# Optimization experiments

Measured on AMD Instinct MI355X. Metric: run time of the kernel, lower is better.

The kernel has to match this reference:

```python
import jax, jax.numpy as jnp
import numpy as np

C = 256
RED = 2
C2 = C // RED


def setup_inputs() -> dict:
    key = jax.random.key(0)
    ks = jax.random.split(key, 6)
    B, H, W = 8, 64, 64
    x = jax.random.normal(ks[0], (B, C, H, W), dtype=jnp.float32)
    # 1x1 convs stored as [out_ch, in_ch] matrices
    W1 = jax.random.normal(ks[1], (C2, C), dtype=jnp.float32) * (1.0 / np.sqrt(C))
    b1 = jax.random.normal(ks[2], (C2,), dtype=jnp.float32) * 0.01
    W2 = jax.random.normal(ks[3], (C, C2), dtype=jnp.float32) * (1.0 / np.sqrt(C2))
    b2 = jax.random.normal(ks[4], (C,), dtype=jnp.float32) * 0.01
    # torch inits scale to zeros; use randn so the residual branch is active
    scale = jax.random.normal(ks[5], (1, C, 1, 1), dtype=jnp.float32)
    return {"x": x, "W1": W1, "b1": b1, "W2": W2, "b2": b2, "scale": scale}


def reference(x, W1, b1, W2, b2, scale):
    B, Cc, H, Wd = x.shape
    # conv1 (1x1): [B,C,H,W] -> [B,C2,H,W]
    y = jnp.einsum('bchw,oc->bohw', x, W1) + b1[None, :, None, None]
    # flatten spatial, move channels last: [B, N, C2]
    y = y.reshape(B, C2, H * Wd).transpose(0, 2, 1)
    # unscaled self-attention over N spatial positions
    att = jax.nn.softmax(jnp.einsum('bmc,bnc->bmn', y, y), axis=-1)  # [B,N,N]
    out = jnp.einsum('bmn,bnc->bmc', att, y)  # [B,N,C2]
    # faithful to torch: raw .view(B,-1,H,W) WITHOUT permuting back
    out = out.reshape(B, C2, H, Wd)
    # conv2 (1x1): [B,C2,H,W] -> [B,C,H,W]
    out = jnp.einsum('bchw,oc->bohw', out, W2) + b2[None, :, None, None]
    return out * scale + x
```

## Files before the change

### kernel.cpp

```cpp
#include <hip/hip_runtime.h>

#define B_  8
#define C_  256
#define C2_ 128
#define N_  4096
#define LOG2E 1.44269504088896f

typedef _Float16 f16;
typedef _Float16 f16x4 __attribute__((ext_vector_type(4)));
typedef _Float16 f16x8 __attribute__((ext_vector_type(8)));
typedef float f32x4  __attribute__((ext_vector_type(4)));

static __device__ __forceinline__ unsigned pk2(float a, float b) {
  return __builtin_bit_cast(unsigned, __builtin_amdgcn_cvt_pkrtz(a, b));
}

static __device__ __forceinline__ void plane16_swap(unsigned a, unsigned b,
                                                    unsigned& r0, unsigned& r1) {
#if __has_builtin(__builtin_amdgcn_permlane16_swap)
  auto r = __builtin_amdgcn_permlane16_swap(a, b, false, false);
  r0 = (unsigned)r[0]; r1 = (unsigned)r[1];
#else
  asm volatile("v_permlane16_swap_b32 %0, %1" : "+v"(a), "+v"(b));
  r0 = a; r1 = b;
#endif
}

static __device__ __forceinline__ void gload16(const void* g, void* l) {
  __builtin_amdgcn_global_load_lds(
      (const __attribute__((address_space(1))) unsigned int*)g,
      (__attribute__((address_space(3))) unsigned int*)l, 16, 0, 0);
}

__global__ __launch_bounds__(256)
void prep_kernel(const float* __restrict__ W1, const float* __restrict__ W2,
                 f16* __restrict__ w1h, f16* __restrict__ w2h)
{
  int i = blockIdx.x * 256 + threadIdx.x;
  w1h[i] = (f16)W1[i];
  w2h[i] = (f16)W2[i];
}

__global__ __launch_bounds__(256, 3)
void conv1_kernel(const float* __restrict__ x,
                  const f16* __restrict__ w1h,
                  const float* __restrict__ b1,
                  f16* __restrict__ Y, f16* __restrict__ Yt)
{
  __shared__ __align__(16) char smem[32768];
  f16* Xh = (f16*)smem;
  f16* Ah = (f16*)(smem + 16384);
  f16* T  = (f16*)smem;

  const int t = threadIdx.x;
  const int w = t >> 6, lane = t & 63, quad = lane >> 4, l16 = lane & 15;
  const int b = blockIdx.x, nt0 = blockIdx.y;

#pragma unroll
  for (int pass = 0; pass < 8; pass++) {
    int c  = (t >> 3) + pass * 32;
    int n4 = t & 7;
    float4 v = *(const float4*)(x + ((long)(b * C_ + c)) * N_ + nt0 * 32 + n4 * 4);
    f16x4 h = {(f16)v.x, (f16)v.y, (f16)v.z, (f16)v.w};
    *(f16x4*)(&Xh[c * 32 + (n4 ^ (c & 7)) * 4]) = h;
  }
  __syncthreads();
#pragma unroll
  for (int pass = 0; pass < 4; pass++) {
    int n  = t & 31;
    int kb = (t >> 5) + pass * 8;
    f16x8 vh;
#pragma unroll
    for (int jj = 0; jj < 8; jj++) {
      int cc = kb * 8 + jj;
      vh[jj] = Xh[cc * 32 + ((n >> 2) ^ (cc & 7)) * 4 + (n & 3)];
    }
    *(f16x8*)(&Ah[n * 256 + (kb ^ (n & 7)) * 8]) = vh;
  }
  __syncthreads();

  f16x8 bh[2][8];
#pragma unroll
  for (int nt = 0; nt < 2; nt++) {
    int c2 = w * 32 + nt * 16 + l16;
#pragma unroll
    for (int ks = 0; ks < 8; ks++)
      bh[nt][ks] = *(const f16x8*)(w1h + c2 * C_ + ks * 32 + quad * 8);
  }

  f32x4 acc[2][2];
#pragma unroll
  for (int i = 0; i < 2; i++)
#pragma unroll
    for (int j = 0; j < 2; j++) acc[i][j] = (f32x4){0.f, 0.f, 0.f, 0.f};

#pragma unroll
  for (int ks = 0; ks < 8; ks++)
#pragma unroll
    for (int mt = 0; mt < 2; mt++) {
      f16x8 ah = *(const f16x8*)(&Ah[(mt * 16 + l16) * 256 + (((ks * 4 + quad) ^ (l16 & 7))) * 8]);
#pragma unroll
      for (int nt = 0; nt < 2; nt++)
        acc[mt][nt] = __builtin_amdgcn_mfma_f32_16x16x32_f16(ah, bh[nt][ks], acc[mt][nt], 0, 0, 0);
    }
  __syncthreads();

#pragma unroll
  for (int nt = 0; nt < 2; nt++) {
    int c2 = w * 32 + nt * 16 + l16;
    float bv = b1[c2];
#pragma unroll
    for (int mt = 0; mt < 2; mt++)
#pragma unroll
      for (int rg = 0; rg < 4; rg++) {
        int n = mt * 16 + quad * 4 + rg;
        T[c2 * 40 + n] = (f16)(acc[mt][nt][rg] + bv);
      }
  }
  __syncthreads();
#pragma unroll
  for (int pass = 0; pass < 2; pass++) {
    int r  = (t >> 2) + pass * 64;
    int c8 = (t & 3) * 8;
    f16x8 v = *(const f16x8*)(&T[r * 40 + c8]);
    *(f16x8*)(Yt + ((long)(b * C2_ + r)) * N_ + nt0 * 32 + c8) = v;
  }
#pragma unroll
  for (int pass = 0; pass < 2; pass++) {
    int row = t & 31;
    int cg  = (t >> 5) + pass * 8;
    f16x8 v;
#pragma unroll
    for (int jj = 0; jj < 8; jj++) v[jj] = T[(cg * 8 + jj) * 40 + row];
    *(f16x8*)(Y + ((long)(b * N_ + nt0 * 32 + row)) * C2_ + cg * 8) = v;
  }
}

__global__ __launch_bounds__(256, 2)
void attn_kernel(const f16* __restrict__ Y, const f16* __restrict__ Yt,
                 f16* __restrict__ Op, float* __restrict__ ls)
{
  __shared__ f16 Ks[2][64 * 128];
  __shared__ f16 Vs[2][128 * 64];
  __shared__ float nsqf[128];

  const int t = threadIdx.x;
  const int w = t >> 6, lane = t & 63, quad = lane >> 4, l16 = lane & 15;
  const int b = blockIdx.x, qt = blockIdx.y, s = blockIdx.z;
  const int ns = gridDim.z;
  const f16* Yb  = Y  + (long)b * N_ * C2_;
  const f16* Ytb = Yt + (long)b * C2_ * N_;
  const int g0 = (s * 64) / ns;
  const int g1 = ((s + 1) * 64) / ns;

  int koff[4], voff[4];
#pragma unroll
  for (int i = 0; i < 4; i++) {
    int p = w + 4 * i;
    int r = 4 * p + (lane >> 4);
    koff[i] = r * C2_ + ((l16 ^ (r & 15)) * 8);
    int d = 8 * p + (lane >> 3);
    voff[i] = d * N_ + (((lane & 7) ^ (d & 7)) * 8);
  }

  f16x8 qf[2][4];
#pragma unroll
  for (int mt = 0; mt < 2; mt++)
#pragma unroll
    for (int ks = 0; ks < 4; ks++)
      qf[mt][ks] = *(const f16x8*)(Yb + (long)(qt * 128 + w * 32 + mt * 16 + l16) * C2_ + ks * 32 + quad * 8);

  {
    int r = t >> 1, half = t & 1;
    float ss = 0.f;
#pragma unroll
    for (int j = 0; j < 8; j++) {
      f16x8 v = *(const f16x8*)(Yb + (long)(qt * 128 + r) * C2_ + half * 64 + j * 8);
#pragma unroll
      for (int e = 0; e < 8; e++) { float f = (float)v[e]; ss = fmaf(f, f, ss); }
    }
    ss += __shfl_xor(ss, 1);
    if (!half) nsqf[r] = ss;
  }

  {
    const int kb0 = g0 * 64;
    const f16* gk = Yb + (long)kb0 * C2_;
    const f16* gv = Ytb + kb0;
#pragma unroll
    for (int i = 0; i < 4; i++) {
      gload16(gk + koff[i], &Ks[0][(w + 4 * i) * 512]);
      gload16(gv + voff[i], &Vs[0][(w + 4 * i) * 512]);
    }
  }
  __syncthreads();

  float nm[2];
  nm[0] = nsqf[w * 32 + l16] * LOG2E;
  nm[1] = nsqf[w * 32 + 16 + l16] * LOG2E;

  f16x8 ones8;
#pragma unroll
  for (int j = 0; j < 8; j++) ones8[j] = (f16)1.0f;

  f32x4 Oa[2][8];
#pragma unroll
  for (int i = 0; i < 2; i++)
#pragma unroll
    for (int j = 0; j < 8; j++) Oa[i][j] = (f32x4){0.f, 0.f, 0.f, 0.f};
  f32x4 lac[2] = {(f32x4){0.f,0.f,0.f,0.f}, (f32x4){0.f,0.f,0.f,0.f}};

  int cur = 0;
#pragma unroll 1
  for (int g = g0; g < g1; g++) {
    if (g + 1 < g1) {
      int nb = (g + 1) * 64;
      const f16* gk = Yb + (long)nb * C2_;
      const f16* gv = Ytb + nb;
#pragma unroll
      for (int i = 0; i < 4; i++) {
        gload16(gk + koff[i], &Ks[cur ^ 1][(w + 4 * i) * 512]);
        gload16(gv + voff[i], &Vs[cur ^ 1][(w + 4 * i) * 512]);
      }
    }

    f32x4 S[4][2];
#pragma unroll
    for (int i = 0; i < 4; i++)
#pragma unroll
      for (int j = 0; j < 2; j++) S[i][j] = (f32x4){0.f, 0.f, 0.f, 0.f};
#pragma unroll
    for (int ks = 0; ks < 4; ks++) {
      f16x8 b0 = *(const f16x8*)(&Ks[cur][(0 * 16 + l16) * 128 + (((ks * 4 + quad) ^ l16)) * 8]);
      f16x8 b1 = *(const f16x8*)(&Ks[cur][(1 * 16 + l16) * 128 + (((ks * 4 + quad) ^ l16)) * 8]);
      __builtin_amdgcn_s_setprio(1);
#pragma unroll
      for (int mt = 0; mt < 2; mt++) {
        S[0][mt] = __builtin_amdgcn_mfma_f32_16x16x32_f16(b0, qf[mt][ks], S[0][mt], 0, 0, 0);
        S[1][mt] = __builtin_amdgcn_mfma_f32_16x16x32_f16(b1, qf[mt][ks], S[1][mt], 0, 0, 0);
      }
      __builtin_amdgcn_s_setprio(0);
    }
#pragma unroll
    for (int ks = 0; ks < 4; ks++) {
      f16x8 b2 = *(const f16x8*)(&Ks[cur][(2 * 16 + l16) * 128 + (((ks * 4 + quad) ^ l16)) * 8]);
      f16x8 b3 = *(const f16x8*)(&Ks[cur][(3 * 16 + l16) * 128 + (((ks * 4 + quad) ^ l16)) * 8]);
      __builtin_amdgcn_s_setprio(1);
#pragma unroll
      for (int mt = 0; mt < 2; mt++) {
        S[2][mt] = __builtin_amdgcn_mfma_f32_16x16x32_f16(b2, qf[mt][ks], S[2][mt], 0, 0, 0);
        S[3][mt] = __builtin_amdgcn_mfma_f32_16x16x32_f16(b3, qf[mt][ks], S[3][mt], 0, 0, 0);
      }
      __builtin_amdgcn_s_setprio(0);
    }

    f16x8 pa0[2];
#pragma unroll
    for (int mt = 0; mt < 2; mt++) {
      float n0 = nm[mt];
      unsigned xa0 = pk2(exp2f(fminf(fmaf(S[0][mt][0], LOG2E, -n0), 11.0f)),
                         exp2f(fminf(fmaf(S[0][mt][1], LOG2E, -n0), 11.0f)));
      unsigned xa1 = pk2(exp2f(fminf(fmaf(S[0][mt][2], LOG2E, -n0), 11.0f)),
                         exp2f(fminf(fmaf(S[0][mt][3], LOG2E, -n0), 11.0f)));
      unsigned xb0 = pk2(exp2f(fminf(fmaf(S[1][mt][0], LOG2E, -n0), 11.0f)),
                         exp2f(fminf(fmaf(S[1][mt][1], LOG2E, -n0), 11.0f)));
      unsigned xb1 = pk2(exp2f(fminf(fmaf(S[1][mt][2], LOG2E, -n0), 11.0f)),
                         exp2f(fminf(fmaf(S[1][mt][3], LOG2E, -n0), 11.0f)));
      union { unsigned u[4]; f16x8 v; } P;
      {
        auto c = __builtin_amdgcn_permlane32_swap(xa0, xb0, false, false);
        plane16_swap((unsigned)c[0], (unsigned)c[1], P.u[0], P.u[2]);
      }
      {
        auto c = __builtin_amdgcn_permlane32_swap(xa1, xb1, false, false);
        plane16_swap((unsigned)c[0], (unsigned)c[1], P.u[1], P.u[3]);
      }
      pa0[mt] = P.v;
    }

    {
      f16x8 vb[8];
#pragma unroll
      for (int dt = 0; dt < 8; dt++)
        vb[dt] = *(const f16x8*)(&Vs[cur][(dt * 16 + l16) * 64 + (((0 * 4 + quad) ^ (l16 & 7))) * 8]);
      __builtin_amdgcn_s_setprio(1);
#pragma unroll
      for (int mt = 0; mt < 2; mt++) {
#pragma unroll
        for (int dt = 0; dt < 8; dt++)
          Oa[mt][dt] = __builtin_amdgcn_mfma_f32_16x16x32_f16(pa0[mt], vb[dt], Oa[mt][dt], 0, 0, 0);
        lac[mt] = __builtin_amdgcn_mfma_f32_16x16x32_f16(pa0[mt], ones8, lac[mt], 0, 0, 0);
      }
      __builtin_amdgcn_s_setprio(0);
    }

    f16x8 pa1[2];
#pragma unroll
    for (int mt = 0; mt < 2; mt++) {
      float n0 = nm[mt];
      unsigned xa0 = pk2(exp2f(fminf(fmaf(S[2][mt][0], LOG2E, -n0), 11.0f)),
                         exp2f(fminf(fmaf(S[2][mt][1], LOG2E, -n0), 11.0f)));
      unsigned xa1 = pk2(exp2f(fminf(fmaf(S[2][mt][2], LOG2E, -n0), 11.0f)),
                         exp2f(fminf(fmaf(S[2][mt][3], LOG2E, -n0), 11.0f)));
      unsigned xb0 = pk2(exp2f(fminf(fmaf(S[3][mt][0], LOG2E, -n0), 11.0f)),
                         exp2f(fminf(fmaf(S[3][mt][1], LOG2E, -n0), 11.0f)));
      unsigned xb1 = pk2(exp2f(fminf(fmaf(S[3][mt][2], LOG2E, -n0), 11.0f)),
                         exp2f(fminf(fmaf(S[3][mt][3], LOG2E, -n0), 11.0f)));
      union { unsigned u[4]; f16x8 v; } P;
      {
        auto c = __builtin_amdgcn_permlane32_swap(xa0, xb0, false, false);
        plane16_swap((unsigned)c[0], (unsigned)c[1], P.u[0], P.u[2]);
      }
      {
        auto c = __builtin_amdgcn_permlane32_swap(xa1, xb1, false, false);
        plane16_swap((unsigned)c[0], (unsigned)c[1], P.u[1], P.u[3]);
      }
      pa1[mt] = P.v;
    }

    {
      f16x8 vb[8];
#pragma unroll
      for (int dt = 0; dt < 8; dt++)
        vb[dt] = *(const f16x8*)(&Vs[cur][(dt * 16 + l16) * 64 + (((1 * 4 + quad) ^ (l16 & 7))) * 8]);
      __builtin_amdgcn_s_setprio(1);
#pragma unroll
      for (int mt = 0; mt < 2; mt++) {
#pragma unroll
        for (int dt = 0; dt < 8; dt++)
          Oa[mt][dt] = __builtin_amdgcn_mfma_f32_16x16x32_f16(pa1[mt], vb[dt], Oa[mt][dt], 0, 0, 0);
        lac[mt] = __builtin_amdgcn_mfma_f32_16x16x32_f16(pa1[mt], ones8, lac[mt], 0, 0, 0);
      }
      __builtin_amdgcn_s_setprio(0);
    }

    __syncthreads();
    cur ^= 1;
  }

  const long rbase = ((long)s * B_ + b) * N_ + qt * 128;
#pragma unroll
  for (int mt = 0; mt < 2; mt++)
#pragma unroll
    for (int rg = 0; rg < 4; rg++) {
      int r = w * 32 + mt * 16 + quad * 4 + rg;
#pragma unroll
      for (int dt = 0; dt < 8; dt++)
        Op[(rbase + r) * C2_ + dt * 16 + l16] = (f16)Oa[mt][dt][rg];
      if (l16 == 0) ls[rbase + r] = lac[mt][rg];
    }
}

__global__ __launch_bounds__(256, 4)
void conv2_kernel(const f16* __restrict__ Op, const float* __restrict__ ls,
                  const f16* __restrict__ w2h,
                  const float* __restrict__ b2,
                  const float* __restrict__ scale,
                  const float* __restrict__ x,
                  float* __restrict__ out, int ns)
{
  __shared__ __align__(16) char smem2[35328];
  f16*   Or   = (f16*)smem2;
  f16*   Bsw  = (f16*)(smem2 + 18432);
  float* invL = (float*)(smem2 + 34816);
  float* Obuf = (float*)smem2;

  const int t = threadIdx.x;
  const int w = t >> 6, lane = t & 63, quad = lane >> 4, l16 = lane & 15;
  const int b = blockIdx.x, pt = blockIdx.y, oh = blockIdx.z;
  const long base0 = (long)b * 524288;

  if (t < 128) {
    int q = t * 32 + (pt >> 1);
    float l = 0.f;
    for (int si = 0; si < ns; si++)
      l += ls[(long)si * 32768 + (long)b * N_ + q];
    invL[t] = 1.0f / fmaxf(l, 1e-20f);
  }
  __syncthreads();

#pragma unroll
  for (int pass = 0; pass < 4; pass++) {
    int j = (t >> 3) + pass * 32;
    int c8 = (t & 7) * 8;
    float fa[8] = {0.f,0.f,0.f,0.f,0.f,0.f,0.f,0.f};
    for (int si = 0; si < ns; si++) {
      f16x8 a = *(const f16x8*)(Op + (long)si * 4194304 + base0 + (long)j * N_ + pt * 64 + c8);
#pragma unroll
      for (int jj = 0; jj < 8; jj++) fa[jj] += (float)a[jj];
    }
    float iv = invL[j];
    f16x8 r;
#pragma unroll
    for (int jj = 0; jj < 8; jj++)
      r[jj] = (f16)(fa[jj] * iv);
    *(f16x8*)(&Or[j * 72 + c8]) = r;
  }
  __syncthreads();
#pragma unroll
  for (int pass = 0; pass < 4; pass++) {
    int p = t & 63;
    int q = (t >> 6) + pass * 4;
    f16x8 vv;
#pragma unroll
    for (int jj = 0; jj < 8; jj++) vv[jj] = Or[(q * 8 + jj) * 72 + p];
    *(f16x8*)(&Bsw[p * 128 + ((q ^ (p & 15))) * 8]) = vv;
  }
  __syncthreads();

  f32x4 acc[2][4];
#pragma unroll
  for (int i = 0; i < 2; i++)
#pragma unroll
    for (int j = 0; j < 4; j++) acc[i][j] = (f32x4){0.f, 0.f, 0.f, 0.f};

#pragma unroll
  for (int ks = 0; ks < 4; ks++) {
    f16x8 bfr[4];
#pragma unroll
    for (int nt = 0; nt < 4; nt++)
      bfr[nt] = *(const f16x8*)(&Bsw[(nt * 16 + l16) * 128 + (((ks * 4 + quad) ^ l16)) * 8]);
#pragma unroll
    for (int mt = 0; mt < 2; mt++) {
      int o = oh * 128 + w * 32 + mt * 16 + l16;
      f16x8 ah = *(const f16x8*)(w2h + o * C2_ + ks * 32 + quad * 8);
#pragma unroll
      for (int nt = 0; nt < 4; nt++)
        acc[mt][nt] = __builtin_amdgcn_mfma_f32_16x16x32_f16(ah, bfr[nt], acc[mt][nt], 0, 0, 0);
    }
  }

  __syncthreads();
#pragma unroll
  for (int mt = 0; mt < 2; mt++)
#pragma unroll
    for (int nt = 0; nt < 4; nt++)
#pragma unroll
      for (int rg = 0; rg < 4; rg++)
        Obuf[(w * 32 + mt * 16 + quad * 4 + rg) * 68 + nt * 16 + l16] = acc[mt][nt][rg];
  __syncthreads();
#pragma unroll
  for (int pass = 0; pass < 8; pass++) {
    int idx = pass * 256 + t;
    int ol  = idx >> 4;
    int p4  = (idx & 15) * 4;
    float4 v = *(const float4*)(&Obuf[ol * 68 + p4]);
    int o = oh * 128 + ol;
    float so = scale[o], bo = b2[o];
    long xo = ((long)b * C_ + o) * N_ + pt * 64 + p4;
    float4 xv = *(const float4*)(x + xo);
    float4 r;
    r.x = (v.x + bo) * so + xv.x;
    r.y = (v.y + bo) * so + xv.y;
    r.z = (v.z + bo) * so + xv.z;
    r.w = (v.w + bo) * so + xv.w;
    *(float4*)(out + xo) = r;
  }
}

extern "C" void kernel_launch(void* const* d_in, const int* in_sizes, int n_in,
                              void* d_out, int out_size, void* d_ws, size_t ws_size,
                              hipStream_t stream) {
  const float* x     = (const float*)d_in[0];
  const float* W1    = (const float*)d_in[1];
  const float* b1    = (const float*)d_in[2];
  const float* W2    = (const float*)d_in[3];
  const float* b2    = (const float*)d_in[4];
  const float* scale = (const float*)d_in[5];
  float* outp = (float*)d_out;

  const size_t NE = (size_t)B_ * N_ * C2_;
  const int ns = 2;

  f16* Y   = (f16*)d_ws;
  f16* Yt  = Y + NE;
  f16* Op  = Yt + NE;
  float* ls = (float*)(Op + (size_t)ns * NE);
  f16* w1h = (f16*)(ls + (size_t)ns * 32768);
  f16* w2h = w1h + 32768;

  prep_kernel <<<dim3(128),       dim3(256), 0, stream>>>(W1, W2, w1h, w2h);
  conv1_kernel<<<dim3(8, 128),    dim3(256), 0, stream>>>(x, w1h, b1, Y, Yt);
  attn_kernel <<<dim3(8, 32, ns), dim3(256), 0, stream>>>(Y, Yt, Op, ls);
  conv2_kernel<<<dim3(8, 64, 2),  dim3(256), 0, stream>>>(Op, ls, w2h, b2, scale, x, outp, ns);
}
```

Before: 208.6 us.

## Software-pipeline QK and PV across key tiles; merge conv2 output halves per block

The attention loop now computes QK^T for tile i while running the PV MFMAs of tile i-1, using stored P fragments. K is loaded one tile ahead and V is loaded for the current tile into alternating buffers, with a drain step after the loop. The aim is to overlap the softmax exp work with matrix-core work. Separately, conv2 loops over both output-channel halves inside one block, so the partial-output merge and transpose are done once instead of twice. This doubles the block's LDS and halves the grid. Register pressure rises in attention, and conv2 occupancy drops.

```diff
diff --git a/kernel.cpp b/kernel.cpp
--- a/kernel.cpp
+++ b/kernel.cpp
@@ -152,6 +152,7 @@
   const f16* Ytb = Yt + (long)b * C2_ * N_;
   const int g0 = (s * 64) / ns;
   const int g1 = ((s + 1) * 64) / ns;
+  const int nt_ = g1 - g0;
 
   int koff[4], voff[4];
 #pragma unroll
@@ -184,14 +185,10 @@
   }
 
   {
-    const int kb0 = g0 * 64;
-    const f16* gk = Yb + (long)kb0 * C2_;
-    const f16* gv = Ytb + kb0;
-#pragma unroll
-    for (int i = 0; i < 4; i++) {
+    const f16* gk = Yb + (long)(g0 * 64) * C2_;
+#pragma unroll
+    for (int i = 0; i < 4; i++)
       gload16(gk + koff[i], &Ks[0][(w + 4 * i) * 512]);
-      gload16(gv + voff[i], &Vs[0][(w + 4 * i) * 512]);
-    }
   }
   __syncthreads();
 
@@ -210,132 +207,109 @@
     for (int j = 0; j < 8; j++) Oa[i][j] = (f32x4){0.f, 0.f, 0.f, 0.f};
   f32x4 lac[2] = {(f32x4){0.f,0.f,0.f,0.f}, (f32x4){0.f,0.f,0.f,0.f}};
 
-  int cur = 0;
+  f16x8 pa_prev[2][2];
+
 #pragma unroll 1
-  for (int g = g0; g < g1; g++) {
-    if (g + 1 < g1) {
-      int nb = (g + 1) * 64;
-      const f16* gk = Yb + (long)nb * C2_;
-      const f16* gv = Ytb + nb;
-#pragma unroll
-      for (int i = 0; i < 4; i++) {
-        gload16(gk + koff[i], &Ks[cur ^ 1][(w + 4 * i) * 512]);
-        gload16(gv + voff[i], &Vs[cur ^ 1][(w + 4 * i) * 512]);
+  for (int i = 0; i < nt_; i++) {
+    const int g = g0 + i;
+    const int kb = i & 1;
+
+    if (i + 1 < nt_) {
+      const f16* gk = Yb + (long)((g + 1) * 64) * C2_;
+#pragma unroll
+      for (int j = 0; j < 4; j++)
+        gload16(gk + koff[j], &Ks[kb ^ 1][(w + 4 * j) * 512]);
+    }
+    {
+      const f16* gv = Ytb + g * 64;
+#pragma unroll
+      for (int j = 0; j < 4; j++)
+        gload16(gv + voff[j], &Vs[kb][(w + 4 * j) * 512]);
+    }
+
+    f32x4 S[4][2];
+#pragma unroll
+    for (int a = 0; a < 4; a++)
+#pragma unroll
+      for (int j = 0; j < 2; j++) S[a][j] = (f32x4){0.f, 0.f, 0.f, 0.f};
+#pragma unroll
+    for (int ks = 0; ks < 4; ks++) {
+      f16x8 bfr[4];
+#pragma unroll
+      for (int nt = 0; nt < 4; nt++)
+        bfr[nt] = *(const f16x8*)(&Ks[kb][(nt * 16 + l16) * 128 + (((ks * 4 + quad) ^ l16)) * 8]);
+      __builtin_amdgcn_s_setprio(1);
+#pragma unroll
+      for (int nt = 0; nt < 4; nt++)
+#pragma unroll
+        for (int mt = 0; mt < 2; mt++)
+          S[nt][mt] = __builtin_amdgcn_mfma_f32_16x16x32_f16(bfr[nt], qf[mt][ks], S[nt][mt], 0, 0, 0);
+      __builtin_amdgcn_s_setprio(0);
+    }
+
+    if (i > 0) {
+#pragma unroll
+      for (int ks2 = 0; ks2 < 2; ks2++) {
+        f16x8 vb[8];
+#pragma unroll
+        for (int dt = 0; dt < 8; dt++)
+          vb[dt] = *(const f16x8*)(&Vs[kb ^ 1][(dt * 16 + l16) * 64 + (((ks2 * 4 + quad) ^ (l16 & 7))) * 8]);
+        __builtin_amdgcn_s_setprio(1);
+#pragma unroll
+        for (int mt = 0; mt < 2; mt++) {
+#pragma unroll
+          for (int dt = 0; dt < 8; dt++)
+            Oa[mt][dt] = __builtin_amdgcn_mfma_f32_16x16x32_f16(pa_prev[ks2][mt], vb[dt], Oa[mt][dt], 0, 0, 0);
+          lac[mt] = __builtin_amdgcn_mfma_f32_16x16x32_f16(pa_prev[ks2][mt], ones8, lac[mt], 0, 0, 0);
+        }
+        __builtin_amdgcn_s_setprio(0);
       }
     }
 
-    f32x4 S[4][2];
-#pragma unroll
-    for (int i = 0; i < 4; i++)
-#pragma unroll
-      for (int j = 0; j < 2; j++) S[i][j] = (f32x4){0.f, 0.f, 0.f, 0.f};
-#pragma unroll
-    for (int ks = 0; ks < 4; ks++) {
-      f16x8 b0 = *(const f16x8*)(&Ks[cur][(0 * 16 + l16) * 128 + (((ks * 4 + quad) ^ l16)) * 8]);
-      f16x8 b1 = *(const f16x8*)(&Ks[cur][(1 * 16 + l16) * 128 + (((ks * 4 + quad) ^ l16)) * 8]);
-      __builtin_amdgcn_s_setprio(1);
+#pragma unroll
+    for (int ks2 = 0; ks2 < 2; ks2++)
 #pragma unroll
       for (int mt = 0; mt < 2; mt++) {
-        S[0][mt] = __builtin_amdgcn_mfma_f32_16x16x32_f16(b0, qf[mt][ks], S[0][mt], 0, 0, 0);
-        S[1][mt] = __builtin_amdgcn_mfma_f32_16x16x32_f16(b1, qf[mt][ks], S[1][mt], 0, 0, 0);
+        float n0 = nm[mt];
+        unsigned xa0 = pk2(exp2f(fminf(fmaf(S[2 * ks2][mt][0], LOG2E, -n0), 11.0f)),
+                           exp2f(fminf(fmaf(S[2 * ks2][mt][1], LOG2E, -n0), 11.0f)));
+        unsigned xa1 = pk2(exp2f(fminf(fmaf(S[2 * ks2][mt][2], LOG2E, -n0), 11.0f)),
+                           exp2f(fminf(fmaf(S[2 * ks2][mt][3], LOG2E, -n0), 11.0f)));
+        unsigned xb0 = pk2(exp2f(fminf(fmaf(S[2 * ks2 + 1][mt][0], LOG2E, -n0), 11.0f)),
+                           exp2f(fminf(fmaf(S[2 * ks2 + 1][mt][1], LOG2E, -n0), 11.0f)));
+        unsigned xb1 = pk2(exp2f(fminf(fmaf(S[2 * ks2 + 1][mt][2], LOG2E, -n0), 11.0f)),
+                           exp2f(fminf(fmaf(S[2 * ks2 + 1][mt][3], LOG2E, -n0), 11.0f)));
+        union { unsigned u[4]; f16x8 v; } P;
+        {
+          auto c = __builtin_amdgcn_permlane32_swap(xa0, xb0, false, false);
+          plane16_swap((unsigned)c[0], (unsigned)c[1], P.u[0], P.u[2]);
+        }
+        {
+          auto c = __builtin_amdgcn_permlane32_swap(xa1, xb1, false, false);
+          plane16_swap((unsigned)c[0], (unsigned)c[1], P.u[1], P.u[3]);
+        }
+        pa_prev[ks2][mt] = P.v;
       }
-      __builtin_amdgcn_s_setprio(0);
-    }
-#pragma unroll
-    for (int ks = 0; ks < 4; ks++) {
-      f16x8 b2 = *(const f16x8*)(&Ks[cur][(2 * 16 + l16) * 128 + (((ks * 4 + quad) ^ l16)) * 8]);
-      f16x8 b3 = *(const f16x8*)(&Ks[cur][(3 * 16 + l16) * 128 + (((ks * 4 + quad) ^ l16)) * 8]);
-      __builtin_amdgcn_s_setprio(1);
+
+    __syncthreads();
+  }
+
+  {
+    const int kb = (nt_ - 1) & 1;
+#pragma unroll
+    for (int ks2 = 0; ks2 < 2; ks2++) {
+      f16x8 vb[8];
+#pragma unroll
+      for (int dt = 0; dt < 8; dt++)
+        vb[dt] = *(const f16x8*)(&Vs[kb][(dt * 16 + l16) * 64 + (((ks2 * 4 + quad) ^ (l16 & 7))) * 8]);
 #pragma unroll
       for (int mt = 0; mt < 2; mt++) {
-        S[2][mt] = __builtin_amdgcn_mfma_f32_16x16x32_f16(b2, qf[mt][ks], S[2][mt], 0, 0, 0);
-        S[3][mt] = __builtin_amdgcn_mfma_f32_16x16x32_f16(b3, qf[mt][ks], S[3][mt], 0, 0, 0);
+#pragma unroll
+        for (int dt = 0; dt < 8; dt++)
+          Oa[mt][dt] = __builtin_amdgcn_mfma_f32_16x16x32_f16(pa_prev[ks2][mt], vb[dt], Oa[mt][dt], 0, 0, 0);
+        lac[mt] = __builtin_amdgcn_mfma_f32_16x16x32_f16(pa_prev[ks2][mt], ones8, lac[mt], 0, 0, 0);
       }
-      __builtin_amdgcn_s_setprio(0);
-    }
-
-    f16x8 pa0[2];
-#pragma unroll
-    for (int mt = 0; mt < 2; mt++) {
-      float n0 = nm[mt];
-      unsigned xa0 = pk2(exp2f(fminf(fmaf(S[0][mt][0], LOG2E, -n0), 11.0f)),
-                         exp2f(fminf(fmaf(S[0][mt][1], LOG2E, -n0), 11.0f)));
-      unsigned xa1 = pk2(exp2f(fminf(fmaf(S[0][mt][2], LOG2E, -n0), 11.0f)),
-                         exp2f(fminf(fmaf(S[0][mt][3], LOG2E, -n0), 11.0f)));
-      unsigned xb0 = pk2(exp2f(fminf(fmaf(S[1][mt][0], LOG2E, -n0), 11.0f)),
-                         exp2f(fminf(fmaf(S[1][mt][1], LOG2E, -n0), 11.0f)));
-      unsigned xb1 = pk2(exp2f(fminf(fmaf(S[1][mt][2], LOG2E, -n0), 11.0f)),
-                         exp2f(fminf(fmaf(S[1][mt][3], LOG2E, -n0), 11.0f)));
-      union { unsigned u[4]; f16x8 v; } P;
-      {
-        auto c = __builtin_amdgcn_permlane32_swap(xa0, xb0, false, false);
-        plane16_swap((unsigned)c[0], (unsigned)c[1], P.u[0], P.u[2]);
-      }
-      {
-        auto c = __builtin_amdgcn_permlane32_swap(xa1, xb1, false, false);
-        plane16_swap((unsigned)c[0], (unsigned)c[1], P.u[1], P.u[3]);
-      }
-      pa0[mt] = P.v;
-    }
-
-    {
-      f16x8 vb[8];
-#pragma unroll
-      for (int dt = 0; dt < 8; dt++)
-        vb[dt] = *(const f16x8*)(&Vs[cur][(dt * 16 + l16) * 64 + (((0 * 4 + quad) ^ (l16 & 7))) * 8]);
-      __builtin_amdgcn_s_setprio(1);
-#pragma unroll
-      for (int mt = 0; mt < 2; mt++) {
-#pragma unroll
-        for (int dt = 0; dt < 8; dt++)
-          Oa[mt][dt] = __builtin_amdgcn_mfma_f32_16x16x32_f16(pa0[mt], vb[dt], Oa[mt][dt], 0, 0, 0);
-        lac[mt] = __builtin_amdgcn_mfma_f32_16x16x32_f16(pa0[mt], ones8, lac[mt], 0, 0, 0);
-      }
-      __builtin_amdgcn_s_setprio(0);
-    }
-
-    f16x8 pa1[2];
-#pragma unroll
-    for (int mt = 0; mt < 2; mt++) {
-      float n0 = nm[mt];
-      unsigned xa0 = pk2(exp2f(fminf(fmaf(S[2][mt][0], LOG2E, -n0), 11.0f)),
-                         exp2f(fminf(fmaf(S[2][mt][1], LOG2E, -n0), 11.0f)));
-      unsigned xa1 = pk2(exp2f(fminf(fmaf(S[2][mt][2], LOG2E, -n0), 11.0f)),
-                         exp2f(fminf(fmaf(S[2][mt][3], LOG2E, -n0), 11.0f)));
-      unsigned xb0 = pk2(exp2f(fminf(fmaf(S[3][mt][0], LOG2E, -n0), 11.0f)),
-                         exp2f(fminf(fmaf(S[3][mt][1], LOG2E, -n0), 11.0f)));
-      unsigned xb1 = pk2(exp2f(fminf(fmaf(S[3][mt][2], LOG2E, -n0), 11.0f)),
-                         exp2f(fminf(fmaf(S[3][mt][3], LOG2E, -n0), 11.0f)));
-      union { unsigned u[4]; f16x8 v; } P;
-      {
-        auto c = __builtin_amdgcn_permlane32_swap(xa0, xb0, false, false);
-        plane16_swap((unsigned)c[0], (unsigned)c[1], P.u[0], P.u[2]);
-      }
-      {
-        auto c = __builtin_amdgcn_permlane32_swap(xa1, xb1, false, false);
-        plane16_swap((unsigned)c[0], (unsigned)c[1], P.u[1], P.u[3]);
-      }
-      pa1[mt] = P.v;
-    }
-
-    {
-      f16x8 vb[8];
-#pragma unroll
-      for (int dt = 0; dt < 8; dt++)
-        vb[dt] = *(const f16x8*)(&Vs[cur][(dt * 16 + l16) * 64 + (((1 * 4 + quad) ^ (l16 & 7))) * 8]);
-      __builtin_amdgcn_s_setprio(1);
-#pragma unroll
-      for (int mt = 0; mt < 2; mt++) {
-#pragma unroll
-        for (int dt = 0; dt < 8; dt++)
-          Oa[mt][dt] = __builtin_amdgcn_mfma_f32_16x16x32_f16(pa1[mt], vb[dt], Oa[mt][dt], 0, 0, 0);
-        lac[mt] = __builtin_amdgcn_mfma_f32_16x16x32_f16(pa1[mt], ones8, lac[mt], 0, 0, 0);
-      }
-      __builtin_amdgcn_s_setprio(0);
-    }
-
-    __syncthreads();
-    cur ^= 1;
+    }
   }
 
   const long rbase = ((long)s * B_ + b) * N_ + qt * 128;
@@ -351,7 +325,7 @@
     }
 }
 
-__global__ __launch_bounds__(256, 4)
+__global__ __launch_bounds__(256, 2)
 void conv2_kernel(const f16* __restrict__ Op, const float* __restrict__ ls,
                   const f16* __restrict__ w2h,
                   const float* __restrict__ b2,
@@ -359,15 +333,15 @@
                   const float* __restrict__ x,
                   float* __restrict__ out, int ns)
 {
-  __shared__ __align__(16) char smem2[35328];
+  __shared__ __align__(16) char smem2[70144];
   f16*   Or   = (f16*)smem2;
   f16*   Bsw  = (f16*)(smem2 + 18432);
   float* invL = (float*)(smem2 + 34816);
-  float* Obuf = (float*)smem2;
+  float* Obuf = (float*)(smem2 + 35328);
 
   const int t = threadIdx.x;
   const int w = t >> 6, lane = t & 63, quad = lane >> 4, l16 = lane & 15;
-  const int b = blockIdx.x, pt = blockIdx.y, oh = blockIdx.z;
+  const int b = blockIdx.x, pt = blockIdx.y;
   const long base0 = (long)b * 524288;
 
   if (t < 128) {
@@ -408,53 +382,56 @@
   }
   __syncthreads();
 
-  f32x4 acc[2][4];
-#pragma unroll
-  for (int i = 0; i < 2; i++)
-#pragma unroll
-    for (int j = 0; j < 4; j++) acc[i][j] = (f32x4){0.f, 0.f, 0.f, 0.f};
-
-#pragma unroll
-  for (int ks = 0; ks < 4; ks++) {
-    f16x8 bfr[4];
-#pragma unroll
-    for (int nt = 0; nt < 4; nt++)
-      bfr[nt] = *(const f16x8*)(&Bsw[(nt * 16 + l16) * 128 + (((ks * 4 + quad) ^ l16)) * 8]);
-#pragma unroll
-    for (int mt = 0; mt < 2; mt++) {
-      int o = oh * 128 + w * 32 + mt * 16 + l16;
-      f16x8 ah = *(const f16x8*)(w2h + o * C2_ + ks * 32 + quad * 8);
+#pragma unroll 1
+  for (int oh = 0; oh < 2; oh++) {
+    f32x4 acc[2][4];
+#pragma unroll
+    for (int i = 0; i < 2; i++)
+#pragma unroll
+      for (int j = 0; j < 4; j++) acc[i][j] = (f32x4){0.f, 0.f, 0.f, 0.f};
+
+#pragma unroll
+    for (int ks = 0; ks < 4; ks++) {
+      f16x8 bfr[4];
 #pragma unroll
       for (int nt = 0; nt < 4; nt++)
-        acc[mt][nt] = __builtin_amdgcn_mfma_f32_16x16x32_f16(ah, bfr[nt], acc[mt][nt], 0, 0, 0);
-    }
-  }
-
-  __syncthreads();
-#pragma unroll
-  for (int mt = 0; mt < 2; mt++)
-#pragma unroll
-    for (int nt = 0; nt < 4; nt++)
-#pragma unroll
-      for (int rg = 0; rg < 4; rg++)
-        Obuf[(w * 32 + mt * 16 + quad * 4 + rg) * 68 + nt * 16 + l16] = acc[mt][nt][rg];
-  __syncthreads();
-#pragma unroll
-  for (int pass = 0; pass < 8; pass++) {
-    int idx = pass * 256 + t;
-    int ol  = idx >> 4;
-    int p4  = (idx & 15) * 4;
-    float4 v = *(const float4*)(&Obuf[ol * 68 + p4]);
-    int o = oh * 128 + ol;
-    float so = scale[o], bo = b2[o];
-    long xo = ((long)b * C_ + o) * N_ + pt * 64 + p4;
-    float4 xv = *(const float4*)(x + xo);
-    float4 r;
-    r.x = (v.x + bo) * so + xv.x;
-    r.y = (v.y + bo) * so + xv.y;
-    r.z = (v.z + bo) * so + xv.z;
-    r.w = (v.w + bo) * so + xv.w;
-    *(float4*)(out + xo) = r;
+        bfr[nt] = *(const f16x8*)(&Bsw[(nt * 16 + l16) * 128 + (((ks * 4 + quad) ^ l16)) * 8]);
+#pragma unroll
+      for (int mt = 0; mt < 2; mt++) {
+        int o = oh * 128 + w * 32 + mt * 16 + l16;
+        f16x8 ah = *(const f16x8*)(w2h + o * C2_ + ks * 32 + quad * 8);
+#pragma unroll
+        for (int nt = 0; nt < 4; nt++)
+          acc[mt][nt] = __builtin_amdgcn_mfma_f32_16x16x32_f16(ah, bfr[nt], acc[mt][nt], 0, 0, 0);
+      }
+    }
+
+    __syncthreads();
+#pragma unroll
+    for (int mt = 0; mt < 2; mt++)
+#pragma unroll
+      for (int nt = 0; nt < 4; nt++)
+#pragma unroll
+        for (int rg = 0; rg < 4; rg++)
+          Obuf[(w * 32 + mt * 16 + quad * 4 + rg) * 68 + nt * 16 + l16] = acc[mt][nt][rg];
+    __syncthreads();
+#pragma unroll
+    for (int pass = 0; pass < 8; pass++) {
+      int idx = pass * 256 + t;
+      int ol  = idx >> 4;
+      int p4  = (idx & 15) * 4;
+      float4 v = *(const float4*)(&Obuf[ol * 68 + p4]);
+      int o = oh * 128 + ol;
+      float so = scale[o], bo = b2[o];
+      long xo = ((long)b * C_ + o) * N_ + pt * 64 + p4;
+      float4 xv = *(const float4*)(x + xo);
+      float4 r;
+      r.x = (v.x + bo) * so + xv.x;
+      r.y = (v.y + bo) * so + xv.y;
+      r.z = (v.z + bo) * so + xv.z;
+      r.w = (v.w + bo) * so + xv.w;
+      *(float4*)(out + xo) = r;
+    }
   }
 }
 
@@ -482,5 +459,5 @@
   prep_kernel <<<dim3(128),       dim3(256), 0, stream>>>(W1, W2, w1h, w2h);
   conv1_kernel<<<dim3(8, 128),    dim3(256), 0, stream>>>(x, w1h, b1, Y, Yt);
   attn_kernel <<<dim3(8, 32, ns), dim3(256), 0, stream>>>(Y, Yt, Op, ls);
-  conv2_kernel<<<dim3(8, 64, 2),  dim3(256), 0, stream>>>(Op, ls, w2h, b2, scale, x, outp, ns);
-}
+  conv2_kernel<<<dim3(8, 64),     dim3(256), 0, stream>>>(Op, ls, w2h, b2, scale, x, outp, ns);
+}
```

Result: faster. 197.8 us (-5.2%).
